# Optimization experiments

Measured on AMD Instinct MI355X. Metric: run time of the kernel, lower is better.

The kernel has to match this reference:

```python
import jax, jax.numpy as jnp
import numpy as np

N, E, IN, OUT, MC, H, C, HID = 50000, 800000, 64, 64, 16, 4, 16, 128
NEG = 0.2   # leaky_relu negative slope
EPS = 1e-5  # BatchNorm eps


def _gcn(x, src, dst, norm, W, b):
    # GCNConv: symmetric-normalized aggregation with self-loops already in (src, dst)
    h = x @ W
    return jax.ops.segment_sum(h[src] * norm[:, None], dst, num_segments=N) + b


def _gat(x, src, dst, W, b, a_s, a_d):
    # GATConv, concat=True: h -> [N, H, C]
    h = (x @ W).reshape(N, H, C)
    e = jax.nn.leaky_relu((h * a_s).sum(-1)[src] + (h * a_d).sum(-1)[dst], NEG)  # [E+N, H]
    m = jax.ops.segment_max(e, dst, num_segments=N)
    p = jnp.exp(e - m[dst])
    alpha = p / jax.ops.segment_sum(p, dst, num_segments=N)[dst]
    out = jax.ops.segment_sum(h[src] * alpha[..., None], dst, num_segments=N)
    return out.reshape(N, H * C) + b


def _bn(x):
    # BatchNorm(affine=False), training stats (biased variance)
    mu = x.mean(0)
    var = x.var(0)
    return (x - mu) / jnp.sqrt(var + EPS)


def _spade(x, mask, src, dst, norm, w0, b0, wg, bg, wb, bb):
    mf = jax.nn.relu(_gcn(mask, src, dst, norm, w0, b0))
    gamma = _gcn(mf, src, dst, norm, wg, bg)
    beta = _gcn(mf, src, dst, norm, wb, bb)
    return _bn(x) * (1.0 + gamma) + beta


def _forward(x, mask, edge_index, params):
    s1, s2, sk, g1, g2, gk = params
    loop = jnp.arange(N, dtype=edge_index.dtype)  # self-loops (GCN & GAT defaults)
    src = jnp.concatenate([edge_index[0], loop])
    dst = jnp.concatenate([edge_index[1], loop])
    deg = jax.ops.segment_sum(jnp.ones(src.shape[0], x.dtype), dst, num_segments=N)
    dinv = jnp.where(deg > 0, jax.lax.rsqrt(deg), 0.0)
    norm = dinv[src] * dinv[dst]
    xm = jax.nn.leaky_relu(_spade(x, mask, src, dst, norm, *s1), NEG)
    xm = _gat(xm, src, dst, *g1)
    xm = jax.nn.leaky_relu(_spade(xm, mask, src, dst, norm, *s2), NEG)
    xm = _gat(xm, src, dst, *g2)
    xs = jax.nn.leaky_relu(_spade(x, mask, src, dst, norm, *sk), NEG)
    xs = _gat(xs, src, dst, *gk)
    return xm + xs


def setup_inputs() -> dict:
    key = jax.random.key(0)
    ks = iter(jax.random.split(key, 40))
    def rn(shape, scale=1.0):
        return jax.random.normal(next(ks), shape, jnp.float32) * scale
    inp = {
        "x": rn((N, IN)),
        "mask": rn((N, MC)),
        "edge_index": jax.random.randint(next(ks), (2, E), 0, N, dtype=jnp.int32),
    }
    for p in ("s1", "s2", "sk"):
        inp[p + "_w0"] = rn((MC, HID), 0.1)
        inp[p + "_b0"] = jnp.zeros(HID, jnp.float32)
        inp[p + "_wg"] = rn((HID, IN), 0.05)
        inp[p + "_bg"] = jnp.zeros(IN, jnp.float32)
        inp[p + "_wb"] = rn((HID, IN), 0.05)
        inp[p + "_bb"] = jnp.zeros(IN, jnp.float32)
    for g, din in (("g1", IN), ("g2", OUT), ("gk", IN)):
        inp[g + "_w"] = rn((din, H * C), 0.1)
        inp[g + "_b"] = jnp.zeros(H * C, jnp.float32)
        inp[g + "_as"] = rn((H, C), 0.1)
        inp[g + "_ad"] = rn((H, C), 0.1)
    return inp


def reference(x, mask, edge_index,
              s1_w0, s1_b0, s1_wg, s1_bg, s1_wb, s1_bb,
              s2_w0, s2_b0, s2_wg, s2_bg, s2_wb, s2_bb,
              sk_w0, sk_b0, sk_wg, sk_bg, sk_wb, sk_bb,
              g1_w, g1_b, g1_as, g1_ad,
              g2_w, g2_b, g2_as, g2_ad,
              gk_w, gk_b, gk_as, gk_ad):
    params = (
        (s1_w0, s1_b0, s1_wg, s1_bg, s1_wb, s1_bb),
        (s2_w0, s2_b0, s2_wg, s2_bg, s2_wb, s2_bb),
        (sk_w0, sk_b0, sk_wg, sk_bg, sk_wb, sk_bb),
        (g1_w, g1_b, g1_as, g1_ad),
        (g2_w, g2_b, g2_as, g2_ad),
        (gk_w, gk_b, gk_as, gk_ad),
    )
    return _forward(x, mask, edge_index, params)
```

## Files before the change

kernel.cpp:

```cpp
#include <hip/hip_runtime.h>
#include <hip/hip_fp16.h>

constexpr int kN   = 50000;
constexpr int kE   = 800000;
constexpr float kNEG = 0.2f;
constexpr float kEPS = 1e-5f;
constexpr int kNB16 = kN / 16;

__device__ __forceinline__ float lrelu(float x) { return x > 0.f ? x : kNEG * x; }

__device__ __forceinline__ void unpack8(int4 raw, float* t) {
    __half2* h = (__half2*)&raw;
    #pragma unroll
    for (int i = 0; i < 4; ++i) { float2 f = __half22float2(h[i]); t[2*i] = f.x; t[2*i+1] = f.y; }
}


__global__ void k_count(const int* __restrict__ ei, int* __restrict__ cnt) {
    int e = blockIdx.x * blockDim.x + threadIdx.x;
    if (e < kE) atomicAdd(&cnt[ei[kE + e]], 1);
}

__global__ void k_scan(const int* __restrict__ cnt, int* __restrict__ rp,
                       float* __restrict__ dinv) {
    __shared__ int wsum[16];
    __shared__ int chunk_base;
    int tid = threadIdx.x, lane = tid & 63, wid = tid >> 6;
    if (tid == 0) chunk_base = 0;
    __syncthreads();
    for (int base = 0; base < kN; base += 1024) {
        int i = base + tid;
        int v = (i < kN) ? cnt[i] : 0;
        if (i < kN) dinv[i] = rsqrtf((float)(v + 1));
        int s = v;
        #pragma unroll
        for (int off = 1; off < 64; off <<= 1) {
            int t = __shfl_up(s, off);
            if (lane >= off) s += t;
        }
        if (lane == 63) wsum[wid] = s;
        __syncthreads();
        if (wid == 0) {
            int t = (lane < 16) ? wsum[lane] : 0;
            #pragma unroll
            for (int off = 1; off < 16; off <<= 1) {
                int u = __shfl_up(t, off);
                if (lane >= off) t += u;
            }
            if (lane < 16) wsum[lane] = t;
        }
        __syncthreads();
        int wbase = (wid > 0) ? wsum[wid - 1] : 0;
        int total = wsum[15];
        int excl = chunk_base + wbase + s - v;
        if (i < kN) rp[i] = excl;
        __syncthreads();
        if (tid == 0) chunk_base += total;
        __syncthreads();
    }
    if (threadIdx.x == 0) rp[kN] = chunk_base;
}

__global__ void k_fill(const int* __restrict__ ei, const int* __restrict__ rp,
                       int* __restrict__ fill, int* __restrict__ col) {
    int e = blockIdx.x * blockDim.x + threadIdx.x;
    if (e < kE) {
        int d = ei[kE + e];
        int pos = rp[d] + atomicAdd(&fill[d], 1);
        col[pos] = ei[e];
    }
}


__global__ void k_combo(const float* __restrict__ mask, const float* __restrict__ x,
                        const float* __restrict__ dinv, const int* __restrict__ rp,
                        const int* __restrict__ col,
                        float* __restrict__ am, float* __restrict__ sraw_x) {
    if (blockIdx.x < kNB16) {
        int node = blockIdx.x * 16 + threadIdx.x / 16;
        int f = threadIdx.x % 16;
        float dv = dinv[node];
        float acc = dv * mask[(size_t)node * 16 + f];
        int b = rp[node], e2 = rp[node + 1];
        for (int i = b; i < e2; ++i) {
            int u = col[i];
            acc += dinv[u] * mask[(size_t)u * 16 + f];
        }
        am[(size_t)node * 16 + f] = dv * acc;
    } else {
        int bb = blockIdx.x - kNB16;
        int f = threadIdx.x % 64, r0 = threadIdx.x / 64;
        float s = 0.f, s2 = 0.f;
        for (int v = bb * 4 + r0; v < kN; v += 256 * 4) {
            float val = x[(size_t)v * 64 + f];
            s += val; s2 += val * val;
        }
        __shared__ float sh[256], sh2[256];
        sh[threadIdx.x] = s; sh2[threadIdx.x] = s2;
        __syncthreads();
        if (threadIdx.x < 64) {
            s  = sh[threadIdx.x]  + sh[threadIdx.x + 64]  + sh[threadIdx.x + 128]  + sh[threadIdx.x + 192];
            s2 = sh2[threadIdx.x] + sh2[threadIdx.x + 64] + sh2[threadIdx.x + 128] + sh2[threadIdx.x + 192];
            atomicAdd(&sraw_x[f], s);
            atomicAdd(&sraw_x[64 + f], s2);
        }
    }
}


__global__ void k_bnstats(const float* __restrict__ x, float* __restrict__ stats) {
    int f = threadIdx.x % 64, r0 = threadIdx.x / 64;
    float s = 0.f, s2 = 0.f;
    for (int v = blockIdx.x * 4 + r0; v < kN; v += gridDim.x * 4) {
        float val = x[(size_t)v * 64 + f];
        s += val; s2 += val * val;
    }
    __shared__ float sh[256], sh2[256];
    sh[threadIdx.x] = s; sh2[threadIdx.x] = s2;
    __syncthreads();
    if (threadIdx.x < 64) {
        s  = sh[threadIdx.x]  + sh[threadIdx.x + 64]  + sh[threadIdx.x + 128]  + sh[threadIdx.x + 192];
        s2 = sh2[threadIdx.x] + sh2[threadIdx.x + 64] + sh2[threadIdx.x + 128] + sh2[threadIdx.x + 192];
        atomicAdd(&stats[f], s);
        atomicAdd(&stats[64 + f], s2);
    }
}


__global__ void k_mf2(const float* __restrict__ am,
                      const float* __restrict__ w0a, const float* __restrict__ b0a,
                      const float* __restrict__ w0b, const float* __restrict__ b0b,
                      const float* __restrict__ dinv,
                      __half* __restrict__ Pa, __half* __restrict__ Pb) {
    int set = blockIdx.x / kNB16;
    int blk = blockIdx.x - set * kNB16;
    const float* w0 = set ? w0b : w0a;
    const float* b0 = set ? b0b : b0a;
    __half* P = set ? Pb : Pa;
    __shared__ float w[16 * 128];
    __shared__ float a[16 * 16];
    int tid = threadIdx.x;
    int n0 = blk * 16;
    {
        const float4* w04 = (const float4*)w0;
        float4* w4 = (float4*)w;
        #pragma unroll
        for (int i = 0; i < 2; ++i) w4[tid + 256 * i] = w04[tid + 256 * i];
        if (tid < 64) {
            const float4* am4 = (const float4*)am;
            int node = n0 + tid / 4;
            ((float4*)a)[tid] = am4[(size_t)node * 4 + (tid & 3)];
        }
    }
    __syncthreads();
    int f = tid % 128, g = tid / 128;
    float bf = b0[f];
    for (int j = 0; j < 8; ++j) {
        int nl = g * 8 + j;
        int node = n0 + nl;
        float acc = bf;
        #pragma unroll
        for (int k = 0; k < 16; ++k) acc += a[nl * 16 + k] * w[k * 128 + f];
        P[(size_t)node * 128 + f] = __float2half(dinv[node] * fmaxf(acc, 0.f));
    }
}


struct SpgatArgs {
    const float* xin; const __half* P;
    const float *wg, *bg, *wb, *bb, *sraw, *W, *as_, *ad_;
    __half* h; float* esed; int eslot;
};

__global__ void k_spgat(SpgatArgs A, SpgatArgs B,
                        const float* __restrict__ dinv, const int* __restrict__ rp,
                        const int* __restrict__ col) {
    SpgatArgs G = (blockIdx.x < kNB16) ? A : B;
    int blk = (blockIdx.x < kNB16) ? blockIdx.x : blockIdx.x - kNB16;
    __shared__ float smem[6144];
    float* a   = smem;
    float* wgs = smem + 2048;
    float* wbs = smem + 4096;
    float* ys  = smem;
    float* ws  = smem + 1024;
    int tid = threadIdx.x;
    int n0 = blk * 16;
    {
        int node = n0 + tid / 16;
        int l = tid & 15;
        const int4* P4 = (const int4*)G.P;
        float dv = dinv[node];
        float acc[8];
        unpack8(P4[(size_t)node * 16 + l], acc);
        int b = rp[node], e2 = rp[node + 1];
        for (int base = b; base < e2; base += 16) {
            int idx = base + l;
            int myu = (idx < e2) ? col[idx] : 0;
            int n = min(16, e2 - base);
            for (int cc = 0; cc < n; ++cc) {
                int u = __shfl(myu, cc, 16);
                float t[8];
                unpack8(P4[(size_t)u * 16 + l], t);
                #pragma unroll
                for (int q = 0; q < 8; ++q) acc[q] += t[q];
            }
        }
        float* dst = a + (tid / 16) * 128 + l * 8;
        ((float4*)dst)[0] = make_float4(dv * acc[0], dv * acc[1], dv * acc[2], dv * acc[3]);
        ((float4*)dst)[1] = make_float4(dv * acc[4], dv * acc[5], dv * acc[6], dv * acc[7]);
    }
    int f = tid % 64, nl = tid / 64;
    float accg[4] = {0,0,0,0}, accb[4] = {0,0,0,0};
    const float4* wg4 = (const float4*)G.wg;
    const float4* wb4 = (const float4*)G.wb;
    for (int c = 0; c < 4; ++c) {
        __syncthreads();
        {
            float4* wgs4 = (float4*)wgs;
            float4* wbs4 = (float4*)wbs;
            #pragma unroll
            for (int i = 0; i < 2; ++i) {
                int idx = tid + 256 * i;
                wgs4[idx] = wg4[c * 512 + idx];
                wbs4[idx] = wb4[c * 512 + idx];
            }
        }
        __syncthreads();
        #pragma unroll
        for (int kk = 0; kk < 32; ++kk) {
            float wgk = wgs[kk * 64 + f], wbk = wbs[kk * 64 + f];
            int k = c * 32 + kk;
            #pragma unroll
            for (int j = 0; j < 4; ++j) {
                float av = a[(j * 4 + nl) * 128 + k];
                accg[j] += av * wgk;
                accb[j] += av * wbk;
            }
        }
    }
    float mu, rstd;
    {
        float s = G.sraw[f], s2 = G.sraw[64 + f];
        mu = s * (1.f / kN);
        rstd = rsqrtf(s2 * (1.f / kN) - mu * mu + kEPS);
    }
    float bgf = G.bg[f], bbf = G.bb[f];
    float yv[4];
    #pragma unroll
    for (int j = 0; j < 4; ++j) {
        int node = n0 + j * 4 + nl;
        float xv = G.xin[(size_t)node * 64 + f];
        float g = accg[j] + bgf, b = accb[j] + bbf;
        yv[j] = lrelu((xv - mu) * rstd * (1.f + g) + b);
    }
    __syncthreads();
    #pragma unroll
    for (int j = 0; j < 4; ++j) ys[(j * 4 + nl) * 64 + f] = yv[j];
    {
        const float4* W4 = (const float4*)G.W;
        float4* ws4 = (float4*)ws;
        #pragma unroll
        for (int i = 0; i < 4; ++i) ws4[tid + 256 * i] = W4[tid + 256 * i];
    }
    __syncthreads();
    float asf = G.as_[f], adf = G.ad_[f];
    float acc[4] = {0,0,0,0};
    for (int k = 0; k < 64; ++k) {
        float w = ws[k * 64 + f];
        #pragma unroll
        for (int j = 0; j < 4; ++j) acc[j] += ys[(j * 4 + nl) * 64 + k] * w;
    }
    #pragma unroll
    for (int j = 0; j < 4; ++j) {
        int node = n0 + j * 4 + nl;
        float hv = acc[j];
        float es = hv * asf, ed = hv * adf;
        #pragma unroll
        for (int off = 1; off < 16; off <<= 1) {
            es += __shfl_xor(es, off);
            ed += __shfl_xor(ed, off);
        }
        G.h[(size_t)node * 64 + f] = __float2half(hv);
        if ((f & 15) == 0) {
            int hh = f >> 4;
            G.esed[node * 16 + G.eslot + hh] = es;
            G.esed[node * 16 + G.eslot + 4 + hh] = ed;
        }
    }
}


__global__ void k_gatagg1(const __half* __restrict__ h, const float* __restrict__ esed,
                          const int* __restrict__ rp, const int* __restrict__ col,
                          const float* __restrict__ bias, float* __restrict__ out) {
    int node = blockIdx.x * 4 + threadIdx.x / 64;
    int lane = threadIdx.x & 63;
    int hh = lane >> 4;
    float edv = esed[node * 16 + 4 + hh];
    float m = lrelu(esed[node * 16 + hh] + edv);
    float d = 1.f;
    float acc = __half2float(h[(size_t)node * 64 + lane]);
    int b = rp[node], e2 = rp[node + 1];
    for (int base = b; base < e2; base += 64) {
        int idx = base + lane;
        int myu = (idx < e2) ? col[idx] : 0;
        int n = min(64, e2 - base);
        for (int cc = 0; cc < n; ++cc) {
            int u = __shfl(myu, cc);
            float e = lrelu(esed[u * 16 + hh] + edv);
            float hu = __half2float(h[(size_t)u * 64 + lane]);
            if (e <= m) {
                float p = __expf(e - m);
                d += p; acc += p * hu;
            } else {
                float s = __expf(m - e);
                d = d * s + 1.f; acc = acc * s + hu; m = e;
            }
        }
    }
    out[(size_t)node * 64 + lane] = acc / d + bias[lane];
}


__global__ void k_gatagg2(const __half* __restrict__ h2, const __half* __restrict__ hk,
                          const float* __restrict__ esed,
                          const int* __restrict__ rp, const int* __restrict__ col,
                          const float* __restrict__ b2, const float* __restrict__ bk,
                          float* __restrict__ out) {
    int node = blockIdx.x * 4 + threadIdx.x / 64;
    int lane = threadIdx.x & 63;
    int hh = lane >> 4;
    float ed2 = esed[node * 16 + 4 + hh];
    float edk = esed[node * 16 + 12 + hh];
    float m2 = lrelu(esed[node * 16 + hh] + ed2);
    float mk = lrelu(esed[node * 16 + 8 + hh] + edk);
    float d2 = 1.f, dk = 1.f;
    float a2 = __half2float(h2[(size_t)node * 64 + lane]);
    float ak = __half2float(hk[(size_t)node * 64 + lane]);
    int b = rp[node], e2 = rp[node + 1];
    for (int base = b; base < e2; base += 64) {
        int idx = base + lane;
        int myu = (idx < e2) ? col[idx] : 0;
        int n = min(64, e2 - base);
        for (int cc = 0; cc < n; ++cc) {
            int u = __shfl(myu, cc);
            float q2 = lrelu(esed[u * 16 + hh] + ed2);
            float qk = lrelu(esed[u * 16 + 8 + hh] + edk);
            float h2u = __half2float(h2[(size_t)u * 64 + lane]);
            float hku = __half2float(hk[(size_t)u * 64 + lane]);
            if (q2 <= m2) { float p = __expf(q2 - m2); d2 += p; a2 += p * h2u; }
            else { float s = __expf(m2 - q2); d2 = d2 * s + 1.f; a2 = a2 * s + h2u; m2 = q2; }
            if (qk <= mk) { float p = __expf(qk - mk); dk += p; ak += p * hku; }
            else { float s = __expf(mk - qk); dk = dk * s + 1.f; ak = ak * s + hku; mk = qk; }
        }
    }
    out[(size_t)node * 64 + lane] = a2 / d2 + b2[lane] + ak / dk + bk[lane];
}


extern "C" void kernel_launch(void* const* d_in, const int* in_sizes, int n_in,
                              void* d_out, int out_size, void* d_ws, size_t ws_size,
                              hipStream_t stream) {
    const float* x    = (const float*)d_in[0];
    const float* mask = (const float*)d_in[1];
    const int*   ei   = (const int*)d_in[2];
    const float* s_w0[3] = {(const float*)d_in[3],  (const float*)d_in[9],  (const float*)d_in[15]};
    const float* s_b0[3] = {(const float*)d_in[4],  (const float*)d_in[10], (const float*)d_in[16]};
    const float* s_wg[3] = {(const float*)d_in[5],  (const float*)d_in[11], (const float*)d_in[17]};
    const float* s_bg[3] = {(const float*)d_in[6],  (const float*)d_in[12], (const float*)d_in[18]};
    const float* s_wb[3] = {(const float*)d_in[7],  (const float*)d_in[13], (const float*)d_in[19]};
    const float* s_bb[3] = {(const float*)d_in[8],  (const float*)d_in[14], (const float*)d_in[20]};
    const float* g_w[3]  = {(const float*)d_in[21], (const float*)d_in[25], (const float*)d_in[29]};
    const float* g_b[3]  = {(const float*)d_in[22], (const float*)d_in[26], (const float*)d_in[30]};
    const float* g_as[3] = {(const float*)d_in[23], (const float*)d_in[27], (const float*)d_in[31]};
    const float* g_ad[3] = {(const float*)d_in[24], (const float*)d_in[28], (const float*)d_in[32]};

    char* base = (char*)d_ws;
    size_t off = 0;
    auto alloc = [&](size_t bytes) -> void* {
        void* p = base + off;
        off = (off + bytes + 255) & ~(size_t)255;
        return p;
    };
    int*   cnt    = (int*)alloc((size_t)kN * 4);
    int*   fill   = (int*)alloc((size_t)kN * 4);
    float* sraw_x = (float*)alloc(128 * 4);
    float* sraw_z = (float*)alloc(128 * 4);
    size_t zero_span = off;
    int*    rp    = (int*)alloc((size_t)(kN + 1) * 4);
    int*    col   = (int*)alloc((size_t)kE * 4);
    float*  dinv  = (float*)alloc((size_t)kN * 4);
    float*  am    = (float*)alloc((size_t)kN * 16 * 4);
    __half* Pa    = (__half*)alloc((size_t)kN * 128 * 2);
    __half* Pb    = (__half*)alloc((size_t)kN * 128 * 2);
    __half* hA    = (__half*)alloc((size_t)kN * 64 * 2);
    __half* hB    = (__half*)alloc((size_t)kN * 64 * 2);
    float*  esed  = (float*)alloc((size_t)kN * 16 * 4);
    float*  z1    = (float*)alloc((size_t)kN * 64 * 4);
    (void)ws_size; (void)n_in; (void)in_sizes; (void)out_size;

    const int EB = (kE + 255) / 256;
    const int GB4 = kN / 4;

    hipMemsetAsync(cnt, 0, zero_span, stream);
    k_count<<<EB, 256, 0, stream>>>(ei, cnt);
    k_scan<<<1, 1024, 0, stream>>>(cnt, rp, dinv);
    k_fill<<<EB, 256, 0, stream>>>(ei, rp, fill, col);
    k_combo<<<kNB16 + 256, 256, 0, stream>>>(mask, x, dinv, rp, col, am, sraw_x);

    k_mf2<<<kNB16, 256, 0, stream>>>(am, s_w0[0], s_b0[0], s_w0[0], s_b0[0], dinv, Pa, Pb);
    {
        SpgatArgs A{x, Pa, s_wg[0], s_bg[0], s_wb[0], s_bb[0], sraw_x,
                    g_w[0], g_as[0], g_ad[0], hA, esed, 0};
        k_spgat<<<kNB16, 256, 0, stream>>>(A, A, dinv, rp, col);
    }
    k_gatagg1<<<GB4, 256, 0, stream>>>(hA, esed, rp, col, g_b[0], z1);

    k_bnstats<<<256, 256, 0, stream>>>(z1, sraw_z);
    k_mf2<<<2 * kNB16, 256, 0, stream>>>(am, s_w0[1], s_b0[1], s_w0[2], s_b0[2], dinv, Pa, Pb);
    {
        SpgatArgs A{z1, Pa, s_wg[1], s_bg[1], s_wb[1], s_bb[1], sraw_z,
                    g_w[1], g_as[1], g_ad[1], hA, esed, 0};
        SpgatArgs B{x,  Pb, s_wg[2], s_bg[2], s_wb[2], s_bb[2], sraw_x,
                    g_w[2], g_as[2], g_ad[2], hB, esed, 8};
        k_spgat<<<2 * kNB16, 256, 0, stream>>>(A, B, dinv, rp, col);
    }
    k_gatagg2<<<GB4, 256, 0, stream>>>(hA, hB, esed, rp, col, g_b[1], g_b[2], (float*)d_out);
}
```

Baseline: 1.204 ms.

## Batch all three mask-GCN aggregations into one gather pass and interleave GAT features

The three SPADE mask-feature projections are now computed in one launch into a single interleaved buffer of 384 halves per node. The first SPADE/GAT kernel gathers all three 128-wide sets in one neighbor traversal and writes the pre-aggregated sets for the second and skip branches. The later kernel then only reads its own node's row instead of walking the graph again. The two branch GAT features are also interleaved as half2, so the final aggregation does one load per neighbor instead of two. The trade is wider per-edge gathers and extra register pressure in the first kernel, plus writing two intermediate buffers.

```diff
diff --git a/kernel.cpp b/kernel.cpp
--- a/kernel.cpp
+++ b/kernel.cpp
@@ -127,16 +127,15 @@
 }
 
 
-__global__ void k_mf2(const float* __restrict__ am,
+__global__ void k_mf3(const float* __restrict__ am,
                       const float* __restrict__ w0a, const float* __restrict__ b0a,
                       const float* __restrict__ w0b, const float* __restrict__ b0b,
-                      const float* __restrict__ dinv,
-                      __half* __restrict__ Pa, __half* __restrict__ Pb) {
+                      const float* __restrict__ w0c, const float* __restrict__ b0c,
+                      const float* __restrict__ dinv, __half* __restrict__ Pall) {
     int set = blockIdx.x / kNB16;
     int blk = blockIdx.x - set * kNB16;
-    const float* w0 = set ? w0b : w0a;
-    const float* b0 = set ? b0b : b0a;
-    __half* P = set ? Pb : Pa;
+    const float* w0 = (set == 0) ? w0a : (set == 1) ? w0b : w0c;
+    const float* b0 = (set == 0) ? b0a : (set == 1) ? b0b : b0c;
     __shared__ float w[16 * 128];
     __shared__ float a[16 * 16];
     int tid = threadIdx.x;
@@ -161,21 +160,159 @@
         float acc = bf;
         #pragma unroll
         for (int k = 0; k < 16; ++k) acc += a[nl * 16 + k] * w[k * 128 + f];
-        P[(size_t)node * 128 + f] = __float2half(dinv[node] * fmaxf(acc, 0.f));
-    }
-}
-
-
-struct SpgatArgs {
-    const float* xin; const __half* P;
+        Pall[(size_t)node * 384 + set * 128 + f] = __float2half(dinv[node] * fmaxf(acc, 0.f));
+    }
+}
+
+
+__global__ void k_spgat1(const float* __restrict__ xin, const __half* __restrict__ Pall,
+                         const float* __restrict__ wg, const float* __restrict__ bg,
+                         const float* __restrict__ wb, const float* __restrict__ bb,
+                         const float* __restrict__ sraw,
+                         const float* __restrict__ W, const float* __restrict__ as_,
+                         const float* __restrict__ ad_,
+                         __half* __restrict__ h1, float* __restrict__ esed,
+                         __half* __restrict__ Qb, __half* __restrict__ Qc,
+                         const float* __restrict__ dinv, const int* __restrict__ rp,
+                         const int* __restrict__ col) {
+    __shared__ float smem[6144];
+    float* a   = smem;
+    float* wgs = smem + 2048;
+    float* wbs = smem + 4096;
+    float* ys  = smem;
+    float* ws  = smem + 1024;
+    int tid = threadIdx.x;
+    int n0 = blockIdx.x * 16;
+    {
+        int node = n0 + tid / 16;
+        int l = tid & 15;
+        const int4* P4 = (const int4*)Pall;
+        float dv = dinv[node];
+        float aa[8], ab[8], ac[8], t[8];
+        unpack8(P4[(size_t)node * 48 + l], aa);
+        unpack8(P4[(size_t)node * 48 + 16 + l], ab);
+        unpack8(P4[(size_t)node * 48 + 32 + l], ac);
+        int b = rp[node], e2 = rp[node + 1];
+        for (int base = b; base < e2; base += 16) {
+            int idx = base + l;
+            int myu = (idx < e2) ? col[idx] : 0;
+            int n = min(16, e2 - base);
+            for (int cc = 0; cc < n; ++cc) {
+                int u = __shfl(myu, cc, 16);
+                size_t r0 = (size_t)u * 48 + l;
+                int4 ra = P4[r0], rb = P4[r0 + 16], rc = P4[r0 + 32];
+                unpack8(ra, t);
+                #pragma unroll
+                for (int q = 0; q < 8; ++q) aa[q] += t[q];
+                unpack8(rb, t);
+                #pragma unroll
+                for (int q = 0; q < 8; ++q) ab[q] += t[q];
+                unpack8(rc, t);
+                #pragma unroll
+                for (int q = 0; q < 8; ++q) ac[q] += t[q];
+            }
+        }
+        float* dst = a + (tid / 16) * 128 + l * 8;
+        ((float4*)dst)[0] = make_float4(dv * aa[0], dv * aa[1], dv * aa[2], dv * aa[3]);
+        ((float4*)dst)[1] = make_float4(dv * aa[4], dv * aa[5], dv * aa[6], dv * aa[7]);
+        int4 r; __half2* hp = (__half2*)&r;
+        #pragma unroll
+        for (int i = 0; i < 4; ++i) hp[i] = __floats2half2_rn(dv * ab[2*i], dv * ab[2*i+1]);
+        ((int4*)Qb)[(size_t)node * 16 + l] = r;
+        #pragma unroll
+        for (int i = 0; i < 4; ++i) hp[i] = __floats2half2_rn(dv * ac[2*i], dv * ac[2*i+1]);
+        ((int4*)Qc)[(size_t)node * 16 + l] = r;
+    }
+    int f = tid % 64, nl = tid / 64;
+    float accg[4] = {0,0,0,0}, accb[4] = {0,0,0,0};
+    const float4* wg4 = (const float4*)wg;
+    const float4* wb4 = (const float4*)wb;
+    for (int c = 0; c < 4; ++c) {
+        __syncthreads();
+        {
+            float4* wgs4 = (float4*)wgs;
+            float4* wbs4 = (float4*)wbs;
+            #pragma unroll
+            for (int i = 0; i < 2; ++i) {
+                int idx = tid + 256 * i;
+                wgs4[idx] = wg4[c * 512 + idx];
+                wbs4[idx] = wb4[c * 512 + idx];
+            }
+        }
+        __syncthreads();
+        #pragma unroll
+        for (int kk = 0; kk < 32; ++kk) {
+            float wgk = wgs[kk * 64 + f], wbk = wbs[kk * 64 + f];
+            int k = c * 32 + kk;
+            #pragma unroll
+            for (int j = 0; j < 4; ++j) {
+                float av = a[(j * 4 + nl) * 128 + k];
+                accg[j] += av * wgk;
+                accb[j] += av * wbk;
+            }
+        }
+    }
+    float mu, rstd;
+    {
+        float s = sraw[f], s2 = sraw[64 + f];
+        mu = s * (1.f / kN);
+        rstd = rsqrtf(s2 * (1.f / kN) - mu * mu + kEPS);
+    }
+    float bgf = bg[f], bbf = bb[f];
+    float yv[4];
+    #pragma unroll
+    for (int j = 0; j < 4; ++j) {
+        int node = n0 + j * 4 + nl;
+        float xv = xin[(size_t)node * 64 + f];
+        float g = accg[j] + bgf, b = accb[j] + bbf;
+        yv[j] = lrelu((xv - mu) * rstd * (1.f + g) + b);
+    }
+    __syncthreads();
+    #pragma unroll
+    for (int j = 0; j < 4; ++j) ys[(j * 4 + nl) * 64 + f] = yv[j];
+    {
+        const float4* W4 = (const float4*)W;
+        float4* ws4 = (float4*)ws;
+        #pragma unroll
+        for (int i = 0; i < 4; ++i) ws4[tid + 256 * i] = W4[tid + 256 * i];
+    }
+    __syncthreads();
+    float asf = as_[f], adf = ad_[f];
+    float acc[4] = {0,0,0,0};
+    for (int k = 0; k < 64; ++k) {
+        float w = ws[k * 64 + f];
+        #pragma unroll
+        for (int j = 0; j < 4; ++j) acc[j] += ys[(j * 4 + nl) * 64 + k] * w;
+    }
+    #pragma unroll
+    for (int j = 0; j < 4; ++j) {
+        int node = n0 + j * 4 + nl;
+        float hv = acc[j];
+        float es = hv * asf, ed = hv * adf;
+        #pragma unroll
+        for (int off = 1; off < 16; off <<= 1) {
+            es += __shfl_xor(es, off);
+            ed += __shfl_xor(ed, off);
+        }
+        h1[(size_t)node * 64 + f] = __float2half(hv);
+        if ((f & 15) == 0) {
+            int hh = f >> 4;
+            esed[node * 16 + hh] = es;
+            esed[node * 16 + 4 + hh] = ed;
+        }
+    }
+}
+
+
+struct Sp2Args {
+    const float* xin; const __half* Q;
     const float *wg, *bg, *wb, *bb, *sraw, *W, *as_, *ad_;
-    __half* h; float* esed; int eslot;
+    int eslot, hoff;
 };
 
-__global__ void k_spgat(SpgatArgs A, SpgatArgs B,
-                        const float* __restrict__ dinv, const int* __restrict__ rp,
-                        const int* __restrict__ col) {
-    SpgatArgs G = (blockIdx.x < kNB16) ? A : B;
+__global__ void k_spgat2(Sp2Args A, Sp2Args B, __half* __restrict__ hall,
+                         float* __restrict__ esed) {
+    Sp2Args G = (blockIdx.x < kNB16) ? A : B;
     int blk = (blockIdx.x < kNB16) ? blockIdx.x : blockIdx.x - kNB16;
     __shared__ float smem[6144];
     float* a   = smem;
@@ -186,28 +323,13 @@
     int tid = threadIdx.x;
     int n0 = blk * 16;
     {
-        int node = n0 + tid / 16;
-        int l = tid & 15;
-        const int4* P4 = (const int4*)G.P;
-        float dv = dinv[node];
-        float acc[8];
-        unpack8(P4[(size_t)node * 16 + l], acc);
-        int b = rp[node], e2 = rp[node + 1];
-        for (int base = b; base < e2; base += 16) {
-            int idx = base + l;
-            int myu = (idx < e2) ? col[idx] : 0;
-            int n = min(16, e2 - base);
-            for (int cc = 0; cc < n; ++cc) {
-                int u = __shfl(myu, cc, 16);
-                float t[8];
-                unpack8(P4[(size_t)u * 16 + l], t);
-                #pragma unroll
-                for (int q = 0; q < 8; ++q) acc[q] += t[q];
-            }
-        }
-        float* dst = a + (tid / 16) * 128 + l * 8;
-        ((float4*)dst)[0] = make_float4(dv * acc[0], dv * acc[1], dv * acc[2], dv * acc[3]);
-        ((float4*)dst)[1] = make_float4(dv * acc[4], dv * acc[5], dv * acc[6], dv * acc[7]);
+        const int4* q4 = (const int4*)G.Q;
+        int node = n0 + tid / 16, h8 = tid & 15;
+        float t[8];
+        unpack8(q4[(size_t)node * 16 + h8], t);
+        float* dst = a + (tid / 16) * 128 + h8 * 8;
+        ((float4*)dst)[0] = make_float4(t[0], t[1], t[2], t[3]);
+        ((float4*)dst)[1] = make_float4(t[4], t[5], t[6], t[7]);
     }
     int f = tid % 64, nl = tid / 64;
     float accg[4] = {0,0,0,0}, accb[4] = {0,0,0,0};
@@ -280,11 +402,11 @@
             es += __shfl_xor(es, off);
             ed += __shfl_xor(ed, off);
         }
-        G.h[(size_t)node * 64 + f] = __float2half(hv);
+        hall[(size_t)node * 128 + 2 * f + G.hoff] = __float2half(hv);
         if ((f & 15) == 0) {
             int hh = f >> 4;
-            G.esed[node * 16 + G.eslot + hh] = es;
-            G.esed[node * 16 + G.eslot + 4 + hh] = ed;
+            esed[node * 16 + G.eslot + hh] = es;
+            esed[node * 16 + G.eslot + 4 + hh] = ed;
         }
     }
 }
@@ -322,21 +444,21 @@
 }
 
 
-__global__ void k_gatagg2(const __half* __restrict__ h2, const __half* __restrict__ hk,
-                          const float* __restrict__ esed,
+__global__ void k_gatagg2(const __half* __restrict__ hall, const float* __restrict__ esed,
                           const int* __restrict__ rp, const int* __restrict__ col,
                           const float* __restrict__ b2, const float* __restrict__ bk,
                           float* __restrict__ out) {
     int node = blockIdx.x * 4 + threadIdx.x / 64;
     int lane = threadIdx.x & 63;
     int hh = lane >> 4;
+    const __half2* h2all = (const __half2*)hall;
     float ed2 = esed[node * 16 + 4 + hh];
     float edk = esed[node * 16 + 12 + hh];
     float m2 = lrelu(esed[node * 16 + hh] + ed2);
     float mk = lrelu(esed[node * 16 + 8 + hh] + edk);
     float d2 = 1.f, dk = 1.f;
-    float a2 = __half2float(h2[(size_t)node * 64 + lane]);
-    float ak = __half2float(hk[(size_t)node * 64 + lane]);
+    float2 hv0 = __half22float2(h2all[(size_t)node * 64 + lane]);
+    float a2 = hv0.x, ak = hv0.y;
     int b = rp[node], e2 = rp[node + 1];
     for (int base = b; base < e2; base += 64) {
         int idx = base + lane;
@@ -346,12 +468,11 @@
             int u = __shfl(myu, cc);
             float q2 = lrelu(esed[u * 16 + hh] + ed2);
             float qk = lrelu(esed[u * 16 + 8 + hh] + edk);
-            float h2u = __half2float(h2[(size_t)u * 64 + lane]);
-            float hku = __half2float(hk[(size_t)u * 64 + lane]);
-            if (q2 <= m2) { float p = __expf(q2 - m2); d2 += p; a2 += p * h2u; }
-            else { float s = __expf(m2 - q2); d2 = d2 * s + 1.f; a2 = a2 * s + h2u; m2 = q2; }
-            if (qk <= mk) { float p = __expf(qk - mk); dk += p; ak += p * hku; }
-            else { float s = __expf(mk - qk); dk = dk * s + 1.f; ak = ak * s + hku; mk = qk; }
+            float2 hv = __half22float2(h2all[(size_t)u * 64 + lane]);
+            if (q2 <= m2) { float p = __expf(q2 - m2); d2 += p; a2 += p * hv.x; }
+            else { float s = __expf(m2 - q2); d2 = d2 * s + 1.f; a2 = a2 * s + hv.x; m2 = q2; }
+            if (qk <= mk) { float p = __expf(qk - mk); dk += p; ak += p * hv.y; }
+            else { float s = __expf(mk - qk); dk = dk * s + 1.f; ak = ak * s + hv.y; mk = qk; }
         }
     }
     out[(size_t)node * 64 + lane] = a2 / d2 + b2[lane] + ak / dk + bk[lane];
@@ -391,10 +512,11 @@
     int*    col   = (int*)alloc((size_t)kE * 4);
     float*  dinv  = (float*)alloc((size_t)kN * 4);
     float*  am    = (float*)alloc((size_t)kN * 16 * 4);
-    __half* Pa    = (__half*)alloc((size_t)kN * 128 * 2);
-    __half* Pb    = (__half*)alloc((size_t)kN * 128 * 2);
-    __half* hA    = (__half*)alloc((size_t)kN * 64 * 2);
-    __half* hB    = (__half*)alloc((size_t)kN * 64 * 2);
+    __half* Pall  = (__half*)alloc((size_t)kN * 384 * 2);
+    __half* Qb    = (__half*)alloc((size_t)kN * 128 * 2);
+    __half* Qc    = (__half*)alloc((size_t)kN * 128 * 2);
+    __half* h1    = (__half*)alloc((size_t)kN * 64 * 2);
+    __half* hall  = (__half*)alloc((size_t)kN * 128 * 2);
     float*  esed  = (float*)alloc((size_t)kN * 16 * 4);
     float*  z1    = (float*)alloc((size_t)kN * 64 * 4);
     (void)ws_size; (void)n_in; (void)in_sizes; (void)out_size;
@@ -408,22 +530,21 @@
     k_fill<<<EB, 256, 0, stream>>>(ei, rp, fill, col);
     k_combo<<<kNB16 + 256, 256, 0, stream>>>(mask, x, dinv, rp, col, am, sraw_x);
 
-    k_mf2<<<kNB16, 256, 0, stream>>>(am, s_w0[0], s_b0[0], s_w0[0], s_b0[0], dinv, Pa, Pb);
-    {
-        SpgatArgs A{x, Pa, s_wg[0], s_bg[0], s_wb[0], s_bb[0], sraw_x,
-                    g_w[0], g_as[0], g_ad[0], hA, esed, 0};
-        k_spgat<<<kNB16, 256, 0, stream>>>(A, A, dinv, rp, col);
-    }
-    k_gatagg1<<<GB4, 256, 0, stream>>>(hA, esed, rp, col, g_b[0], z1);
+    k_mf3<<<3 * kNB16, 256, 0, stream>>>(am, s_w0[0], s_b0[0], s_w0[1], s_b0[1],
+                                         s_w0[2], s_b0[2], dinv, Pall);
+
+    k_spgat1<<<kNB16, 256, 0, stream>>>(x, Pall, s_wg[0], s_bg[0], s_wb[0], s_bb[0], sraw_x,
+                                        g_w[0], g_as[0], g_ad[0], h1, esed, Qb, Qc,
+                                        dinv, rp, col);
+    k_gatagg1<<<GB4, 256, 0, stream>>>(h1, esed, rp, col, g_b[0], z1);
 
     k_bnstats<<<256, 256, 0, stream>>>(z1, sraw_z);
-    k_mf2<<<2 * kNB16, 256, 0, stream>>>(am, s_w0[1], s_b0[1], s_w0[2], s_b0[2], dinv, Pa, Pb);
-    {
-        SpgatArgs A{z1, Pa, s_wg[1], s_bg[1], s_wb[1], s_bb[1], sraw_z,
-                    g_w[1], g_as[1], g_ad[1], hA, esed, 0};
-        SpgatArgs B{x,  Pb, s_wg[2], s_bg[2], s_wb[2], s_bb[2], sraw_x,
-                    g_w[2], g_as[2], g_ad[2], hB, esed, 8};
-        k_spgat<<<2 * kNB16, 256, 0, stream>>>(A, B, dinv, rp, col);
-    }
-    k_gatagg2<<<GB4, 256, 0, stream>>>(hA, hB, esed, rp, col, g_b[1], g_b[2], (float*)d_out);
-}
+    {
+        Sp2Args A{z1, Qb, s_wg[1], s_bg[1], s_wb[1], s_bb[1], sraw_z,
+                  g_w[1], g_as[1], g_ad[1], 0, 0};
+        Sp2Args B{x,  Qc, s_wg[2], s_bg[2], s_wb[2], s_bb[2], sraw_x,
+                  g_w[2], g_as[2], g_ad[2], 8, 1};
+        k_spgat2<<<2 * kNB16, 256, 0, stream>>>(A, B, hall, esed);
+    }
+    k_gatagg2<<<GB4, 256, 0, stream>>>(hall, esed, rp, col, g_b[1], g_b[2], (float*)d_out);
+}
```

New measurement: 1.233 ms. 1.02x slower.
